# Kernel optimization log

Measured on AMD Instinct MI355X. Metric: run time of the kernel, lower is better.

Reference implementation:

```python
import jax, jax.numpy as jnp
import numpy as np

N, E, IN, HID, HEADS, EDIM, LAT = 10000, 160000, 20, 256, 4, 3, 1024


def gat(x, ei, ea, W, a_src, a_dst, We, a_e, b, H, C):
    # PyG GATConv, eval mode. ei: [2,E], ea: [E,edge_dim]
    n = x.shape[0]
    s, d = ei[0], ei[1]
    # add_self_loops with fill_value='mean': self-loop attr = mean of incoming edge attrs
    cnt = jax.ops.segment_sum(jnp.ones_like(s, jnp.float32), d, num_segments=n)
    loop_ea = jax.ops.segment_sum(ea, d, num_segments=n) / jnp.maximum(cnt, 1.0)[:, None]
    ar = jnp.arange(n, dtype=s.dtype)
    s = jnp.concatenate([s, ar])
    d = jnp.concatenate([d, ar])
    ea = jnp.concatenate([ea, loop_ea], axis=0)
    h = (x @ W).reshape(n, H, C)                       # [n,H,C]
    al_s = jnp.einsum('nhc,hc->nh', h, a_src)
    al_d = jnp.einsum('nhc,hc->nh', h, a_dst)
    e = (ea @ We).reshape(-1, H, C)                    # [E',H,C]
    al_e = jnp.einsum('ehc,hc->eh', e, a_e)
    alpha = jax.nn.leaky_relu(al_s[s] + al_d[d] + al_e, 0.2)  # [E',H]
    m = jax.ops.segment_max(alpha, d, num_segments=n)
    ex = jnp.exp(alpha - m[d])
    ssum = jax.ops.segment_sum(ex, d, num_segments=n)
    alpha = ex / (ssum[d] + 1e-16)
    out = jax.ops.segment_sum(h[s] * alpha[:, :, None], d, num_segments=n)
    return out.reshape(n, H * C) + b


def ln(x, g, b, eps=1e-5):
    m = x.mean(-1, keepdims=True)
    v = ((x - m) ** 2).mean(-1, keepdims=True)
    return g * (x - m) / jnp.sqrt(v + eps) + b


def setup_inputs() -> dict:
    key = jax.random.key(0)
    ks = jax.random.split(key, 16)
    sc = 0.05
    HC = HID * HEADS  # 1024
    return {
        'x': jax.random.normal(ks[0], (N, IN), jnp.float32),
        'edge_attr': jax.random.normal(ks[1], (E, EDIM), jnp.float32),
        'W1': jax.random.normal(ks[2], (IN, HC), jnp.float32) * sc,
        'a_src1': jax.random.normal(ks[3], (HEADS, HID), jnp.float32) * sc,
        'a_dst1': jax.random.normal(ks[4], (HEADS, HID), jnp.float32) * sc,
        'We1': jax.random.normal(ks[5], (EDIM, HC), jnp.float32) * sc,
        'a_e1': jax.random.normal(ks[6], (HEADS, HID), jnp.float32) * sc,
        'b1': jnp.zeros((HC,), jnp.float32),
        'g1': jnp.ones((HC,), jnp.float32),
        'be1': jnp.zeros((HC,), jnp.float32),
        'W2': jax.random.normal(ks[7], (HC, HID), jnp.float32) * sc,
        'a_src2': jax.random.normal(ks[8], (1, HID), jnp.float32) * sc,
        'a_dst2': jax.random.normal(ks[9], (1, HID), jnp.float32) * sc,
        'We2': jax.random.normal(ks[10], (EDIM, HID), jnp.float32) * sc,
        'a_e2': jax.random.normal(ks[11], (1, HID), jnp.float32) * sc,
        'b2': jnp.zeros((HID,), jnp.float32),
        'g2': jnp.ones((HID,), jnp.float32),
        'be2': jnp.zeros((HID,), jnp.float32),
        'Wfc': jax.random.normal(ks[12], (2 * HID, LAT), jnp.float32) * sc,
        'bfc': jnp.zeros((LAT,), jnp.float32),
        'gf': jnp.ones((LAT,), jnp.float32),
        'bf': jnp.zeros((LAT,), jnp.float32),
        'edge_index': jax.random.randint(ks[13], (2, E), 0, N, jnp.int32),
    }


def reference(x, edge_attr, W1, a_src1, a_dst1, We1, a_e1, b1, g1, be1,
              W2, a_src2, a_dst2, We2, a_e2, b2, g2, be2,
              Wfc, bfc, gf, bf, edge_index):
    h = jax.nn.elu(gat(x, edge_index, edge_attr, W1, a_src1, a_dst1, We1, a_e1, b1, HEADS, HID))
    h = ln(h, g1, be1)
    h = jax.nn.elu(gat(h, edge_index, edge_attr, W2, a_src2, a_dst2, We2, a_e2, b2, 1, HID))
    h = ln(h, g2, be2)
    x_mean = h.mean(axis=0)   # global_mean_pool, batch all zeros
    x_max = h.max(axis=0)     # global_max_pool
    g = jnp.concatenate([x_mean, x_max])[None, :]  # [1, 2*HID]
    out = ln(jax.nn.relu(g @ Wfc + bfc), gf, bf)   # [1, LAT]
    return out
```

## Files before the change

kernel.cpp:

```cpp
#include <hip/hip_runtime.h>
#include <hip/hip_bf16.h>

#define NN   10000
#define NE   160000
#define NEP  170000
#define IND  20
#define HIDD 256
#define NH   4
#define HCD  1024
#define LATD 1024
#define MPAD 10112
#define NREP 32

typedef __attribute__((ext_vector_type(8))) short short8v;
typedef __attribute__((ext_vector_type(4))) float f32x4;

__device__ __forceinline__ unsigned pk2(float a, float b) {
    union { __hip_bfloat16 h; unsigned short s; } x, y;
    x.h = __float2bfloat16(a); y.h = __float2bfloat16(b);
    return (unsigned)x.s | ((unsigned)y.s << 16);
}

__device__ __forceinline__ float block_reduce_sum1(float v, float* sm) {
    #pragma unroll
    for (int o = 32; o > 0; o >>= 1) v += __shfl_xor(v, o, 64);
    int wid = threadIdx.x >> 6, lane = threadIdx.x & 63, nw = blockDim.x >> 6;
    if (lane == 0) sm[wid] = v;
    __syncthreads();
    float r = 0.f;
    for (int i = 0; i < nw; i++) r += sm[i];
    __syncthreads();
    return r;
}

__global__ void k_prep(const float* __restrict__ W1, const float* __restrict__ as1,
                       const float* __restrict__ ad1, const float* __restrict__ We1,
                       const float* __restrict__ ae1, const float* __restrict__ We2,
                       const float* __restrict__ ae2, const float* __restrict__ W2,
                       float* __restrict__ prm, __hip_bfloat16* __restrict__ Bt,
                       __hip_bfloat16* __restrict__ w1b) {
    int bid = blockIdx.x, t = threadIdx.x;
    if (bid < 64) {
        __shared__ float sm[64][65];
        int k0 = (bid & 15) * 64, c0 = (bid >> 4) * 64;
        #pragma unroll
        for (int i = 0; i < 16; i++) {
            int idx = i * 256 + t;
            int r = idx >> 6, c = idx & 63;
            sm[r][c] = W2[(size_t)(k0 + r) * 256 + c0 + c];
        }
        __syncthreads();
        int c = t >> 2, kq = t & 3;
        unsigned int out[8];
        #pragma unroll
        for (int j = 0; j < 8; j++)
            out[j] = pk2(sm[kq * 16 + 2*j][c], sm[kq * 16 + 2*j + 1][c]);
        unsigned int* dst = (unsigned int*)(Bt + (size_t)(c0 + c) * 1024 + k0 + kq * 16);
        *(uint4*)dst = make_uint4(out[0], out[1], out[2], out[3]);
        *(uint4*)(dst + 4) = make_uint4(out[4], out[5], out[6], out[7]);
    } else if (bid == 64) {
        if (t < 80) {
            int i = t >> 2, h = t & 3; float s = 0.f;
            for (int c = 0; c < HIDD; c++) s += W1[i*HCD + h*HIDD + c] * as1[h*HIDD + c];
            prm[t] = s;
        } else if (t < 160) {
            int u = t - 80; int i = u >> 2, h = u & 3; float s = 0.f;
            for (int c = 0; c < HIDD; c++) s += W1[i*HCD + h*HIDD + c] * ad1[h*HIDD + c];
            prm[t] = s;
        } else if (t < 172) {
            int u = t - 160; int j = u >> 2, h = u & 3; float s = 0.f;
            for (int c = 0; c < HIDD; c++) s += We1[j*HCD + h*HIDD + c] * ae1[h*HIDD + c];
            prm[t] = s;
        } else if (t < 175) {
            int j = t - 172; float s = 0.f;
            for (int c = 0; c < HIDD; c++) s += We2[j*HIDD + c] * ae2[c];
            prm[t] = s;
        }
    } else {
        int base = (bid - 65) * 2560;
        #pragma unroll
        for (int r = 0; r < 10; r++) {
            int id = base + r * 256 + t;
            w1b[id] = __float2bfloat16(W1[id]);
        }
    }
}

__global__ void k_pre1(const int* __restrict__ ei, const float* __restrict__ ea,
                       const float* __restrict__ x, const float* __restrict__ prm,
                       float* __restrict__ cnt, float* __restrict__ lea3,
                       float* __restrict__ al1) {
    int e = blockIdx.x * 256 + threadIdx.x;
    if (e < NE) {
        int d = ei[NE + e];
        atomicAdd(&cnt[d], 1.0f);
        atomicAdd(&lea3[d*3+0], ea[e*3+0]);
        atomicAdd(&lea3[d*3+1], ea[e*3+1]);
        atomicAdd(&lea3[d*3+2], ea[e*3+2]);
    }
    if (e < NN) {
        int v = e;
        float xr[IND];
        #pragma unroll
        for (int i = 0; i < IND; i++) xr[i] = x[v * IND + i];
        #pragma unroll
        for (int h = 0; h < NH; h++) {
            float s = 0.f, d2 = 0.f;
            #pragma unroll
            for (int i = 0; i < IND; i++) { s += xr[i] * prm[i*4 + h]; d2 += xr[i] * prm[80 + i*4 + h]; }
            al1[v*8 + h] = s;
            al1[v*8 + 4 + h] = d2;
        }
    }
}

__global__ void k_scan(const float* __restrict__ cnt, int* __restrict__ offs) {
    __shared__ int sm[1024];
    int t = threadIdx.x;
    int base = t * 10;
    int loc[10]; int s = 0;
    if (t < 1000) {
        #pragma unroll
        for (int i = 0; i < 10; i++) { loc[i] = s; s += (int)cnt[base + i] + 1; }
    }
    sm[t] = (t < 1000) ? s : 0;
    __syncthreads();
    for (int o = 1; o < 1024; o <<= 1) {
        int x = (t >= o) ? sm[t - o] : 0;
        __syncthreads();
        sm[t] += x;
        __syncthreads();
    }
    int pre = (t > 0) ? sm[t - 1] : 0;
    if (t < 1000) {
        #pragma unroll
        for (int i = 0; i < 10; i++) offs[base + i] = pre + loc[i];
    }
    if (t == 1023) offs[NN] = sm[1023];
}

__global__ void k_edge1(const int* __restrict__ ei, const float* __restrict__ ea,
                        const float* __restrict__ cnt, const float* __restrict__ lea3,
                        const float* __restrict__ al1, const float* __restrict__ prm,
                        const int* __restrict__ offs, int* __restrict__ fill1,
                        int* __restrict__ csrs, float* __restrict__ cex1,
                        float* __restrict__ elog2) {
    int e = blockIdx.x * 256 + threadIdx.x;
    if (e >= NEP) return;
    int s, d; float e0, e1, e2;
    if (e < NE) {
        s = ei[e]; d = ei[NE + e];
        e0 = ea[e*3]; e1 = ea[e*3+1]; e2 = ea[e*3+2];
    } else {
        int v = e - NE; s = v; d = v;
        float ic = 1.f / fmaxf(cnt[v], 1.0f);
        e0 = lea3[v*3] * ic; e1 = lea3[v*3+1] * ic; e2 = lea3[v*3+2] * ic;
    }
    int slot = offs[d] + atomicAdd(&fill1[d], 1);
    csrs[slot] = s;
    elog2[slot] = e0*prm[172] + e1*prm[173] + e2*prm[174];
    float ex[4];
    #pragma unroll
    for (int h = 0; h < NH; h++) {
        float le = e0 * prm[160 + h] + e1 * prm[164 + h] + e2 * prm[168 + h];
        float lg = al1[s*8 + h] + al1[d*8 + 4 + h] + le;
        lg = lg > 0.f ? lg : 0.2f * lg;
        ex[h] = expf(lg);
    }
    *(float4*)(cex1 + (size_t)slot * 4) = make_float4(ex[0], ex[1], ex[2], ex[3]);
}

__global__ void __launch_bounds__(256)
k_agg1x(const int* __restrict__ offs, const int* __restrict__ csrs,
        const float* __restrict__ cex1, const float* __restrict__ x,
        const __hip_bfloat16* __restrict__ w1b, const float* __restrict__ b1,
        const float* __restrict__ g1, const float* __restrict__ be1,
        __hip_bfloat16* __restrict__ h1b) {
    __shared__ float xs[4][4][20];
    int l = threadIdx.x & 63, wid = threadIdx.x >> 6;
    int v = blockIdx.x * 4 + wid;
    int beg = offs[v], end = offs[v + 1];
    int half = l >> 5, lx = l & 31;
    float4 ps = make_float4(0.f, 0.f, 0.f, 0.f);
    float ac0 = 0.f, ac1 = 0.f, ac2 = 0.f, ac3 = 0.f;
    for (int j = beg; j < end; j += 64) {
        int nb = end - j; if (nb > 64) nb = 64;
        int jl = j + l;
        bool valid = jl < end;
        int sidx = csrs[valid ? jl : (end - 1)];
        float4 av = valid ? *(const float4*)(cex1 + (size_t)jl * 4)
                          : make_float4(0.f, 0.f, 0.f, 0.f);
        ps.x += av.x; ps.y += av.y; ps.z += av.z; ps.w += av.w;
        for (int u = 0; u < nb; u += 2) {
            int e = u + half;
            int s  = __shfl(sidx, e, 64);
            float w0 = __shfl(av.x, e, 64);
            float w1v = __shfl(av.y, e, 64);
            float w2 = __shfl(av.z, e, 64);
            float w3 = __shfl(av.w, e, 64);
            float xv = (lx < IND) ? x[(size_t)s * IND + lx] : 0.f;
            ac0 += w0 * xv; ac1 += w1v * xv; ac2 += w2 * xv; ac3 += w3 * xv;
        }
    }
    ac0 += __shfl_xor(ac0, 32, 64);
    ac1 += __shfl_xor(ac1, 32, 64);
    ac2 += __shfl_xor(ac2, 32, 64);
    ac3 += __shfl_xor(ac3, 32, 64);
    #pragma unroll
    for (int o = 1; o <= 32; o <<= 1) {
        ps.x += __shfl_xor(ps.x, o, 64);
        ps.y += __shfl_xor(ps.y, o, 64);
        ps.z += __shfl_xor(ps.z, o, 64);
        ps.w += __shfl_xor(ps.w, o, 64);
    }
    if (l < IND) {
        xs[wid][0][l] = ac0; xs[wid][1][l] = ac1;
        xs[wid][2][l] = ac2; xs[wid][3][l] = ac3;
    }
    __syncthreads();
    int hh = l >> 4;
    float invh = 1.f / ((hh == 0 ? ps.x : hh == 1 ? ps.y : hh == 2 ? ps.z : ps.w) + 1e-16f);
    float xreg[IND];
    #pragma unroll
    for (int i = 0; i < IND; i++) xreg[i] = xs[wid][hh][i];
    float vv[16];
    #pragma unroll
    for (int c = 0; c < 16; c++) vv[c] = 0.f;
    #pragma unroll
    for (int i = 0; i < IND; i++) {
        const uint4* wp = (const uint4*)(w1b + (size_t)i * HCD + 16 * l);
        uint4 wa = wp[0], wb = wp[1];
        float xi = xreg[i];
        unsigned wd[8] = {wa.x, wa.y, wa.z, wa.w, wb.x, wb.y, wb.z, wb.w};
        #pragma unroll
        for (int q = 0; q < 8; q++) {
            vv[2*q]   += xi * __uint_as_float(wd[q] << 16);
            vv[2*q+1] += xi * __uint_as_float(wd[q] & 0xffff0000u);
        }
    }
    const float4* b4 = (const float4*)(b1 + 16 * l);
    float lsum = 0.f;
    #pragma unroll
    for (int q = 0; q < 4; q++) {
        float4 bb = b4[q];
        float xv;
        xv = vv[4*q+0] * invh + bb.x; xv = xv > 0.f ? xv : expm1f(xv); vv[4*q+0] = xv; lsum += xv;
        xv = vv[4*q+1] * invh + bb.y; xv = xv > 0.f ? xv : expm1f(xv); vv[4*q+1] = xv; lsum += xv;
        xv = vv[4*q+2] * invh + bb.z; xv = xv > 0.f ? xv : expm1f(xv); vv[4*q+2] = xv; lsum += xv;
        xv = vv[4*q+3] * invh + bb.w; xv = xv > 0.f ? xv : expm1f(xv); vv[4*q+3] = xv; lsum += xv;
    }
    #pragma unroll
    for (int o = 1; o <= 32; o <<= 1) lsum += __shfl_xor(lsum, o, 64);
    float mu = lsum * (1.f / 1024.f);
    float q2 = 0.f;
    #pragma unroll
    for (int i = 0; i < 16; i++) { float dv = vv[i] - mu; q2 += dv * dv; }
    #pragma unroll
    for (int o = 1; o <= 32; o <<= 1) q2 += __shfl_xor(q2, o, 64);
    float rstd = rsqrtf(q2 * (1.f / 1024.f) + 1e-5f);
    const float4* g4 = (const float4*)(g1 + 16 * l);
    const float4* e4 = (const float4*)(be1 + 16 * l);
    unsigned ou[8];
    #pragma unroll
    for (int q = 0; q < 4; q++) {
        float4 gg = g4[q], ee = e4[q];
        float y0 = gg.x * (vv[4*q+0] - mu) * rstd + ee.x;
        float y1 = gg.y * (vv[4*q+1] - mu) * rstd + ee.y;
        float y2 = gg.z * (vv[4*q+2] - mu) * rstd + ee.z;
        float y3 = gg.w * (vv[4*q+3] - mu) * rstd + ee.w;
        ou[2*q]   = pk2(y0, y1);
        ou[2*q+1] = pk2(y2, y3);
    }
    uint4* dst = (uint4*)(h1b + (size_t)v * HCD + 16 * l);
    dst[0] = make_uint4(ou[0], ou[1], ou[2], ou[3]);
    dst[1] = make_uint4(ou[4], ou[5], ou[6], ou[7]);
}

__global__ void __launch_bounds__(256)
k_gemm2m(const __hip_bfloat16* __restrict__ A, const __hip_bfloat16* __restrict__ Bt,
         __hip_bfloat16* __restrict__ h2b) {
    __shared__ uint4 As4[256];
    char* As = (char*)As4;
    int t = threadIdx.x, l = t & 63, w = t >> 6;
    int m0 = blockIdx.x * 32;
    int srow = t >> 3, skc = t & 7;
    const __hip_bfloat16* gA = A + (size_t)(m0 + srow) * 1024 + skc * 8;
    int wbyte = (srow * 128 + skc * 16) ^ ((srow & 7) << 4);
    int r0 = l & 15, g = l >> 4;
    int ra[2][2];
    #pragma unroll
    for (int m = 0; m < 2; m++)
        #pragma unroll
        for (int kk = 0; kk < 2; kk++) {
            int r = r0 + m * 16;
            ra[m][kk] = (r * 128 + kk * 64 + g * 16) ^ ((r & 7) << 4);
        }
    const __hip_bfloat16* gB = Bt + (size_t)(w * 64 + r0) * 1024 + g * 8;
    f32x4 acc[2][4];
    #pragma unroll
    for (int m = 0; m < 2; m++)
        #pragma unroll
        for (int n = 0; n < 4; n++) acc[m][n] = (f32x4){0.f,0.f,0.f,0.f};
    uint4 sreg = *(const uint4*)gA;
    for (int it = 0; it < 16; ++it) {
        *(uint4*)(As + wbyte) = sreg;
        __syncthreads();
        if (it < 15) sreg = *(const uint4*)(gA + (it + 1) * 64);
        int k0 = it * 64;
        short8v bfr[4][2];
        #pragma unroll
        for (int n = 0; n < 4; n++)
            #pragma unroll
            for (int kk = 0; kk < 2; kk++)
                bfr[n][kk] = *(const short8v*)(gB + (size_t)n * 16 * 1024 + k0 + kk * 32);
        short8v afr[2][2];
        #pragma unroll
        for (int m = 0; m < 2; m++)
            #pragma unroll
            for (int kk = 0; kk < 2; kk++)
                afr[m][kk] = *(const short8v*)(As + ra[m][kk]);
        #pragma unroll
        for (int kk = 0; kk < 2; kk++)
            #pragma unroll
            for (int m = 0; m < 2; m++)
                #pragma unroll
                for (int n = 0; n < 4; n++)
                    acc[m][n] = __builtin_amdgcn_mfma_f32_16x16x32_bf16(afr[m][kk], bfr[n][kk], acc[m][n], 0, 0, 0);
        __syncthreads();
    }
    #pragma unroll
    for (int m = 0; m < 2; m++) {
        #pragma unroll
        for (int r = 0; r < 4; r++) {
            int row = m0 + m * 16 + g * 4 + r;
            if (row < NN) {
                #pragma unroll
                for (int n = 0; n < 4; n++) {
                    int col = w * 64 + n * 16 + r0;
                    h2b[(size_t)row * HIDD + col] = __float2bfloat16(acc[m][n][r]);
                }
            }
        }
    }
}

__global__ void __launch_bounds__(256)
k_al2(const __hip_bfloat16* __restrict__ h2b, const float* __restrict__ as2,
      const float* __restrict__ ad2, float* __restrict__ al2) {
    int l = threadIdx.x & 63;
    int v = blockIdx.x * 4 + (threadIdx.x >> 6);
    uint2 p = ((const uint2*)h2b)[(size_t)v * 64 + l];
    float f0 = __uint_as_float(p.x << 16), f1 = __uint_as_float(p.x & 0xffff0000u);
    float f2 = __uint_as_float(p.y << 16), f3 = __uint_as_float(p.y & 0xffff0000u);
    float4 sa = ((const float4*)as2)[l];
    float4 da = ((const float4*)ad2)[l];
    float s = f0*sa.x + f1*sa.y + f2*sa.z + f3*sa.w;
    float d = f0*da.x + f1*da.y + f2*da.z + f3*da.w;
    #pragma unroll
    for (int o = 1; o <= 32; o <<= 1) { s += __shfl_xor(s, o, 64); d += __shfl_xor(d, o, 64); }
    if (l == 0) { al2[v*2] = s; al2[v*2+1] = d; }
}

__global__ void __launch_bounds__(256)
k_agg2(const int* __restrict__ offs, const int* __restrict__ csrs,
       const float* __restrict__ elog2, const float* __restrict__ al2,
       const __hip_bfloat16* __restrict__ h2b, const float* __restrict__ b2,
       const float* __restrict__ g2, const float* __restrict__ be2,
       float* __restrict__ gsum, unsigned* __restrict__ gmaxU) {
    __shared__ float smS[4][256];
    int l = threadIdx.x & 63, w = threadIdx.x >> 6;
    int v = blockIdx.x * 4 + w;
    int beg = offs[v], end = offs[v + 1];
    float ald = al2[2*v + 1];
    float a0 = 0.f, a1 = 0.f, a2 = 0.f, a3 = 0.f, ps = 0.f;
    const uint2* hU = (const uint2*)h2b;
    for (int j = beg; j < end; j += 64) {
        int nb = end - j; if (nb > 64) nb = 64;
        int jl = j + l;
        bool valid = jl < end;
        int sidx = csrs[valid ? jl : (end - 1)];
        float wv = 0.f;
        if (valid) {
            float lg = al2[2*sidx] + ald + elog2[jl];
            lg = lg > 0.f ? lg : 0.2f * lg;
            wv = expf(lg);
        }
        ps += wv;
        for (int u = 0; u < nb; u += 2) {
            int s0 = __shfl(sidx, u, 64);
            int s1 = __shfl(sidx, u + 1, 64);
            float w0 = __shfl(wv, u, 64);
            float w1 = __shfl(wv, u + 1, 64);
            uint2 p = hU[(size_t)s0 * 64 + l];
            uint2 q = hU[(size_t)s1 * 64 + l];
            a0 += w0 * __uint_as_float(p.x << 16);
            a1 += w0 * __uint_as_float(p.x & 0xffff0000u);
            a2 += w0 * __uint_as_float(p.y << 16);
            a3 += w0 * __uint_as_float(p.y & 0xffff0000u);
            a0 += w1 * __uint_as_float(q.x << 16);
            a1 += w1 * __uint_as_float(q.x & 0xffff0000u);
            a2 += w1 * __uint_as_float(q.y << 16);
            a3 += w1 * __uint_as_float(q.y & 0xffff0000u);
        }
    }
    #pragma unroll
    for (int o = 1; o <= 32; o <<= 1) ps += __shfl_xor(ps, o, 64);
    float inv = 1.f / (ps + 1e-16f);
    float4 bb = ((const float4*)b2)[l];
    float v0 = a0 * inv + bb.x, v1 = a1 * inv + bb.y, v2 = a2 * inv + bb.z, v3 = a3 * inv + bb.w;
    v0 = v0 > 0.f ? v0 : expm1f(v0);
    v1 = v1 > 0.f ? v1 : expm1f(v1);
    v2 = v2 > 0.f ? v2 : expm1f(v2);
    v3 = v3 > 0.f ? v3 : expm1f(v3);
    float lsum = v0 + v1 + v2 + v3;
    #pragma unroll
    for (int o = 1; o <= 32; o <<= 1) lsum += __shfl_xor(lsum, o, 64);
    float mu = lsum * (1.f / 256.f);
    float q2 = (v0-mu)*(v0-mu) + (v1-mu)*(v1-mu) + (v2-mu)*(v2-mu) + (v3-mu)*(v3-mu);
    #pragma unroll
    for (int o = 1; o <= 32; o <<= 1) q2 += __shfl_xor(q2, o, 64);
    float rstd = rsqrtf(q2 * (1.f / 256.f) + 1e-5f);
    float4 gg = ((const float4*)g2)[l];
    float4 ee = ((const float4*)be2)[l];
    float4 outv;
    outv.x = gg.x * (v0 - mu) * rstd + ee.x;
    outv.y = gg.y * (v1 - mu) * rstd + ee.y;
    outv.z = gg.z * (v2 - mu) * rstd + ee.z;
    outv.w = gg.w * (v3 - mu) * rstd + ee.w;
    *((float4*)&smS[w][4 * l]) = outv;
    __syncthreads();
    int t = threadIdx.x;
    int rep = blockIdx.x & (NREP - 1);
    float s = smS[0][t] + smS[1][t] + smS[2][t] + smS[3][t];
    float m = fmaxf(fmaxf(smS[0][t], smS[1][t]), fmaxf(smS[2][t], smS[3][t]));
    atomicAdd(&gsum[rep * 256 + t], s);
    unsigned b = __float_as_uint(m);
    unsigned k = (b & 0x80000000u) ? ~b : (b | 0x80000000u);
    atomicMax(&gmaxU[rep * 256 + t], k);
}

__global__ void k_gvec(const float* __restrict__ gsum, const unsigned* __restrict__ gmaxU,
                       float* __restrict__ gvec) {
    int t = threadIdx.x;
    float s = 0.f; unsigned km = 0u;
    #pragma unroll
    for (int r = 0; r < NREP; r++) {
        s += gsum[r * 256 + t];
        unsigned k = gmaxU[r * 256 + t];
        km = k > km ? k : km;
    }
    gvec[t] = s * (1.f / (float)NN);
    unsigned b = (km & 0x80000000u) ? (km & 0x7fffffffu) : ~km;
    gvec[256 + t] = __uint_as_float(b);
}

__global__ void k_fc(const float* __restrict__ gvec, const float* __restrict__ Wfc,
                     const float* __restrict__ bfc, float* __restrict__ fcp) {
    int c = blockIdx.x * 128 + threadIdx.x;
    float acc = bfc[c];
    for (int i = 0; i < 512; i++) acc += gvec[i] * Wfc[i * LATD + c];
    fcp[c] = fmaxf(acc, 0.f);
}

__global__ void k_out(const float* __restrict__ fcp, const float* __restrict__ gf,
                      const float* __restrict__ bf, float* __restrict__ outp) {
    __shared__ float sm[16];
    int t = threadIdx.x;
    float v = fcp[t];
    float mu = block_reduce_sum1(v, sm) * (1.f / 1024.f);
    float dv = v - mu;
    float var = block_reduce_sum1(dv * dv, sm) * (1.f / 1024.f);
    float rstd = rsqrtf(var + 1e-5f);
    outp[t] = gf[t] * dv * rstd + bf[t];
}

extern "C" void kernel_launch(void* const* d_in, const int* in_sizes, int n_in,
                              void* d_out, int out_size, void* d_ws, size_t ws_size,
                              hipStream_t stream) {
    const float* x      = (const float*)d_in[0];
    const float* ea     = (const float*)d_in[1];
    const float* W1     = (const float*)d_in[2];
    const float* a_src1 = (const float*)d_in[3];
    const float* a_dst1 = (const float*)d_in[4];
    const float* We1    = (const float*)d_in[5];
    const float* a_e1   = (const float*)d_in[6];
    const float* b1     = (const float*)d_in[7];
    const float* g1     = (const float*)d_in[8];
    const float* be1    = (const float*)d_in[9];
    const float* W2     = (const float*)d_in[10];
    const float* a_src2 = (const float*)d_in[11];
    const float* a_dst2 = (const float*)d_in[12];
    const float* We2    = (const float*)d_in[13];
    const float* a_e2   = (const float*)d_in[14];
    const float* b2     = (const float*)d_in[15];
    const float* g2     = (const float*)d_in[16];
    const float* be2    = (const float*)d_in[17];
    const float* Wfc    = (const float*)d_in[18];
    const float* bfc    = (const float*)d_in[19];
    const float* gf     = (const float*)d_in[20];
    const float* bf     = (const float*)d_in[21];
    const int*   ei     = (const int*)d_in[22];
    float* outp = (float*)d_out;

    char* p = (char*)d_ws;
    auto alloc = [&](size_t bytes) -> char* {
        char* r = p;
        p += (bytes + 255) & ~(size_t)255;
        return r;
    };
    float* cnt     = (float*)alloc((size_t)NN * 4);
    float* lea3    = (float*)alloc((size_t)NN * 3 * 4);
    int*   fill1   = (int*)  alloc((size_t)NN * 4);
    float* gsum    = (float*)alloc((size_t)NREP * 256 * 4);
    unsigned* gmaxU= (unsigned*)alloc((size_t)NREP * 256 * 4);
    size_t zbytes  = (size_t)((char*)gmaxU + (size_t)NREP*256*4 - (char*)cnt);
    float* prm     = (float*)alloc(256 * 4);
    float* al1     = (float*)alloc((size_t)NN * 8 * 4);
    float* al2     = (float*)alloc((size_t)NN * 2 * 4);
    int*   offs    = (int*)  alloc((size_t)(NN + 1) * 4);
    int*   csrs    = (int*)  alloc((size_t)NEP * 4);
    float* cex1    = (float*)alloc((size_t)NEP * 4 * 4);
    float* elog2   = (float*)alloc((size_t)NEP * 4);
    __hip_bfloat16* w1b = (__hip_bfloat16*)alloc((size_t)IND * HCD * 2);
    __hip_bfloat16* h1b = (__hip_bfloat16*)alloc((size_t)MPAD * HCD * 2);
    __hip_bfloat16* w2t = (__hip_bfloat16*)alloc((size_t)HIDD * HCD * 2);
    __hip_bfloat16* h2b = (__hip_bfloat16*)alloc((size_t)NN * HIDD * 2);
    float* gvec    = (float*)alloc(512 * 4);
    float* fcp     = (float*)alloc(1024 * 4);

    hipMemsetAsync(cnt, 0, zbytes, stream);

    k_prep<<<73, 256, 0, stream>>>(W1, a_src1, a_dst1, We1, a_e1, We2, a_e2, W2,
                                   prm, w2t, w1b);
    k_pre1<<<(NE + 255) / 256, 256, 0, stream>>>(ei, ea, x, prm, cnt, lea3, al1);
    k_scan<<<1, 1024, 0, stream>>>(cnt, offs);
    k_edge1<<<(NEP + 255) / 256, 256, 0, stream>>>(ei, ea, cnt, lea3, al1, prm, offs,
                                                   fill1, csrs, cex1, elog2);
    k_agg1x<<<NN / 4, 256, 0, stream>>>(offs, csrs, cex1, x, w1b, b1, g1, be1, h1b);
    k_gemm2m<<<313, 256, 0, stream>>>(h1b, w2t, h2b);
    k_al2<<<NN / 4, 256, 0, stream>>>(h2b, a_src2, a_dst2, al2);
    k_agg2<<<NN / 4, 256, 0, stream>>>(offs, csrs, elog2, al2, h2b, b2, g2, be2,
                                       gsum, gmaxU);
    k_gvec<<<1, 256, 0, stream>>>(gsum, gmaxU, gvec);
    k_fc<<<8, 128, 0, stream>>>(gvec, Wfc, bfc, fcp);
    k_out<<<1, 1024, 0, stream>>>(fcp, gf, bf, outp);
}
```

Baseline: 318.2 us.

## Restructure layer aggregations and split final FC across blocks

Layer-1 aggregation now gathers neighbor features with 8 edges per wave in parallel and has each block compute the 20x1024 projection for 4 nodes sharing the same weight loads. Layer-2 aggregation uses one 256-thread block per node, staging edge weights and indices in shared memory. Global pooling atomics are spread over more replicas to cut contention. The final FC is split along K across 32 blocks with atomic accumulation, moving bias and ReLU into the output kernel. This trades more blocks and more block-level syncs for better parallelism and reuse.

```diff
diff --git a/kernel.cpp b/kernel.cpp
--- a/kernel.cpp
+++ b/kernel.cpp
@@ -10,7 +10,7 @@
 #define HCD  1024
 #define LATD 1024
 #define MPAD 10112
-#define NREP 32
+#define NREP 128
 
 typedef __attribute__((ext_vector_type(8))) short short8v;
 typedef __attribute__((ext_vector_type(4))) float f32x4;
@@ -31,6 +31,25 @@
     for (int i = 0; i < nw; i++) r += sm[i];
     __syncthreads();
     return r;
+}
+
+__device__ __forceinline__ void block_reduce_sum4(float* v, float* sm) {
+    #pragma unroll
+    for (int h = 0; h < 4; h++) {
+        #pragma unroll
+        for (int o = 32; o > 0; o >>= 1) v[h] += __shfl_xor(v[h], o, 64);
+    }
+    int wid = threadIdx.x >> 6, lane = threadIdx.x & 63, nw = blockDim.x >> 6;
+    if (lane == 0) {
+        sm[wid*4+0] = v[0]; sm[wid*4+1] = v[1]; sm[wid*4+2] = v[2]; sm[wid*4+3] = v[3];
+    }
+    __syncthreads();
+    float r[4] = {0.f, 0.f, 0.f, 0.f};
+    for (int i = 0; i < nw; i++) {
+        r[0] += sm[i*4+0]; r[1] += sm[i*4+1]; r[2] += sm[i*4+2]; r[3] += sm[i*4+3];
+    }
+    __syncthreads();
+    v[0] = r[0]; v[1] = r[1]; v[2] = r[2]; v[3] = r[3];
 }
 
 __global__ void k_prep(const float* __restrict__ W1, const float* __restrict__ as1,
@@ -171,109 +190,106 @@
 }
 
 __global__ void __launch_bounds__(256)
-k_agg1x(const int* __restrict__ offs, const int* __restrict__ csrs,
+k_agg1y(const int* __restrict__ offs, const int* __restrict__ csrs,
         const float* __restrict__ cex1, const float* __restrict__ x,
         const __hip_bfloat16* __restrict__ w1b, const float* __restrict__ b1,
         const float* __restrict__ g1, const float* __restrict__ be1,
         __hip_bfloat16* __restrict__ h1b) {
-    __shared__ float xs[4][4][20];
-    int l = threadIdx.x & 63, wid = threadIdx.x >> 6;
-    int v = blockIdx.x * 4 + wid;
-    int beg = offs[v], end = offs[v + 1];
-    int half = l >> 5, lx = l & 31;
-    float4 ps = make_float4(0.f, 0.f, 0.f, 0.f);
-    float ac0 = 0.f, ac1 = 0.f, ac2 = 0.f, ac3 = 0.f;
-    for (int j = beg; j < end; j += 64) {
-        int nb = end - j; if (nb > 64) nb = 64;
-        int jl = j + l;
-        bool valid = jl < end;
-        int sidx = csrs[valid ? jl : (end - 1)];
-        float4 av = valid ? *(const float4*)(cex1 + (size_t)jl * 4)
-                          : make_float4(0.f, 0.f, 0.f, 0.f);
-        ps.x += av.x; ps.y += av.y; ps.z += av.z; ps.w += av.w;
-        for (int u = 0; u < nb; u += 2) {
-            int e = u + half;
-            int s  = __shfl(sidx, e, 64);
-            float w0 = __shfl(av.x, e, 64);
-            float w1v = __shfl(av.y, e, 64);
-            float w2 = __shfl(av.z, e, 64);
-            float w3 = __shfl(av.w, e, 64);
-            float xv = (lx < IND) ? x[(size_t)s * IND + lx] : 0.f;
-            ac0 += w0 * xv; ac1 += w1v * xv; ac2 += w2 * xv; ac3 += w3 * xv;
-        }
-    }
-    ac0 += __shfl_xor(ac0, 32, 64);
-    ac1 += __shfl_xor(ac1, 32, 64);
-    ac2 += __shfl_xor(ac2, 32, 64);
-    ac3 += __shfl_xor(ac3, 32, 64);
-    #pragma unroll
-    for (int o = 1; o <= 32; o <<= 1) {
-        ps.x += __shfl_xor(ps.x, o, 64);
-        ps.y += __shfl_xor(ps.y, o, 64);
-        ps.z += __shfl_xor(ps.z, o, 64);
-        ps.w += __shfl_xor(ps.w, o, 64);
-    }
-    if (l < IND) {
-        xs[wid][0][l] = ac0; xs[wid][1][l] = ac1;
-        xs[wid][2][l] = ac2; xs[wid][3][l] = ac3;
+    __shared__ float xsn[4][NH][20];
+    __shared__ float smr[16];
+    int t = threadIdx.x, l = t & 63, n0 = t >> 6;
+    int v4 = blockIdx.x * 4;
+    {
+        int v = v4 + n0;
+        int beg = offs[v], end = offs[v + 1];
+        int e = l >> 3, fs = l & 7;
+        float acc[4][3] = {{0.f,0.f,0.f},{0.f,0.f,0.f},{0.f,0.f,0.f},{0.f,0.f,0.f}};
+        float psa[4] = {0.f, 0.f, 0.f, 0.f};
+        for (int j0 = beg; j0 < end; j0 += 8) {
+            int jl = j0 + e;
+            bool valid = jl < end;
+            int s = csrs[valid ? jl : beg];
+            float4 a4 = valid ? *(const float4*)(cex1 + (size_t)jl * 4)
+                              : make_float4(0.f, 0.f, 0.f, 0.f);
+            psa[0] += a4.x; psa[1] += a4.y; psa[2] += a4.z; psa[3] += a4.w;
+            #pragma unroll
+            for (int k = 0; k < 3; k++) {
+                int fi = fs * 3 + k;
+                float xv = (fi < IND) ? x[(size_t)s * IND + fi] : 0.f;
+                acc[0][k] += a4.x * xv; acc[1][k] += a4.y * xv;
+                acc[2][k] += a4.z * xv; acc[3][k] += a4.w * xv;
+            }
+        }
+        #pragma unroll
+        for (int o = 8; o <= 32; o <<= 1) {
+            #pragma unroll
+            for (int h = 0; h < 4; h++) {
+                psa[h] += __shfl_xor(psa[h], o, 64);
+                #pragma unroll
+                for (int k = 0; k < 3; k++) acc[h][k] += __shfl_xor(acc[h][k], o, 64);
+            }
+        }
+        if (e == 0) {
+            #pragma unroll
+            for (int h = 0; h < 4; h++) {
+                float inv = 1.f / (psa[h] + 1e-16f);
+                #pragma unroll
+                for (int k = 0; k < 3; k++) {
+                    int fi = fs * 3 + k;
+                    if (fi < IND) xsn[n0][h][fi] = acc[h][k] * inv;
+                }
+            }
+        }
     }
     __syncthreads();
-    int hh = l >> 4;
-    float invh = 1.f / ((hh == 0 ? ps.x : hh == 1 ? ps.y : hh == 2 ? ps.z : ps.w) + 1e-16f);
-    float xreg[IND];
-    #pragma unroll
-    for (int i = 0; i < IND; i++) xreg[i] = xs[wid][hh][i];
-    float vv[16];
-    #pragma unroll
-    for (int c = 0; c < 16; c++) vv[c] = 0.f;
+    int hh = t >> 6;
+    float vv[4][4] = {{0.f,0.f,0.f,0.f},{0.f,0.f,0.f,0.f},{0.f,0.f,0.f,0.f},{0.f,0.f,0.f,0.f}};
     #pragma unroll
     for (int i = 0; i < IND; i++) {
-        const uint4* wp = (const uint4*)(w1b + (size_t)i * HCD + 16 * l);
-        uint4 wa = wp[0], wb = wp[1];
-        float xi = xreg[i];
-        unsigned wd[8] = {wa.x, wa.y, wa.z, wa.w, wb.x, wb.y, wb.z, wb.w};
-        #pragma unroll
-        for (int q = 0; q < 8; q++) {
-            vv[2*q]   += xi * __uint_as_float(wd[q] << 16);
-            vv[2*q+1] += xi * __uint_as_float(wd[q] & 0xffff0000u);
-        }
-    }
-    const float4* b4 = (const float4*)(b1 + 16 * l);
-    float lsum = 0.f;
-    #pragma unroll
-    for (int q = 0; q < 4; q++) {
-        float4 bb = b4[q];
-        float xv;
-        xv = vv[4*q+0] * invh + bb.x; xv = xv > 0.f ? xv : expm1f(xv); vv[4*q+0] = xv; lsum += xv;
-        xv = vv[4*q+1] * invh + bb.y; xv = xv > 0.f ? xv : expm1f(xv); vv[4*q+1] = xv; lsum += xv;
-        xv = vv[4*q+2] * invh + bb.z; xv = xv > 0.f ? xv : expm1f(xv); vv[4*q+2] = xv; lsum += xv;
-        xv = vv[4*q+3] * invh + bb.w; xv = xv > 0.f ? xv : expm1f(xv); vv[4*q+3] = xv; lsum += xv;
-    }
-    #pragma unroll
-    for (int o = 1; o <= 32; o <<= 1) lsum += __shfl_xor(lsum, o, 64);
-    float mu = lsum * (1.f / 1024.f);
-    float q2 = 0.f;
-    #pragma unroll
-    for (int i = 0; i < 16; i++) { float dv = vv[i] - mu; q2 += dv * dv; }
-    #pragma unroll
-    for (int o = 1; o <= 32; o <<= 1) q2 += __shfl_xor(q2, o, 64);
-    float rstd = rsqrtf(q2 * (1.f / 1024.f) + 1e-5f);
-    const float4* g4 = (const float4*)(g1 + 16 * l);
-    const float4* e4 = (const float4*)(be1 + 16 * l);
-    unsigned ou[8];
-    #pragma unroll
-    for (int q = 0; q < 4; q++) {
-        float4 gg = g4[q], ee = e4[q];
-        float y0 = gg.x * (vv[4*q+0] - mu) * rstd + ee.x;
-        float y1 = gg.y * (vv[4*q+1] - mu) * rstd + ee.y;
-        float y2 = gg.z * (vv[4*q+2] - mu) * rstd + ee.z;
-        float y3 = gg.w * (vv[4*q+3] - mu) * rstd + ee.w;
-        ou[2*q]   = pk2(y0, y1);
-        ou[2*q+1] = pk2(y2, y3);
-    }
-    uint4* dst = (uint4*)(h1b + (size_t)v * HCD + 16 * l);
-    dst[0] = make_uint4(ou[0], ou[1], ou[2], ou[3]);
-    dst[1] = make_uint4(ou[4], ou[5], ou[6], ou[7]);
+        uint2 wd = *(const uint2*)(w1b + (size_t)i * HCD + 4 * t);
+        float w0 = __uint_as_float(wd.x << 16);
+        float w1 = __uint_as_float(wd.x & 0xffff0000u);
+        float w2 = __uint_as_float(wd.y << 16);
+        float w3 = __uint_as_float(wd.y & 0xffff0000u);
+        #pragma unroll
+        for (int n = 0; n < 4; n++) {
+            float xi = xsn[n][hh][i];
+            vv[n][0] += xi * w0; vv[n][1] += xi * w1;
+            vv[n][2] += xi * w2; vv[n][3] += xi * w3;
+        }
+    }
+    float4 bb = ((const float4*)b1)[t];
+    float ls[4];
+    #pragma unroll
+    for (int n = 0; n < 4; n++) {
+        float s0, s1, s2, s3;
+        s0 = vv[n][0] + bb.x; s0 = s0 > 0.f ? s0 : expm1f(s0);
+        s1 = vv[n][1] + bb.y; s1 = s1 > 0.f ? s1 : expm1f(s1);
+        s2 = vv[n][2] + bb.z; s2 = s2 > 0.f ? s2 : expm1f(s2);
+        s3 = vv[n][3] + bb.w; s3 = s3 > 0.f ? s3 : expm1f(s3);
+        vv[n][0] = s0; vv[n][1] = s1; vv[n][2] = s2; vv[n][3] = s3;
+        ls[n] = s0 + s1 + s2 + s3;
+    }
+    block_reduce_sum4(ls, smr);
+    float mu[4], q2[4];
+    #pragma unroll
+    for (int n = 0; n < 4; n++) {
+        mu[n] = ls[n] * (1.f / 1024.f);
+        float d0 = vv[n][0]-mu[n], d1 = vv[n][1]-mu[n], d2 = vv[n][2]-mu[n], d3 = vv[n][3]-mu[n];
+        q2[n] = d0*d0 + d1*d1 + d2*d2 + d3*d3;
+    }
+    block_reduce_sum4(q2, smr);
+    float4 gg = ((const float4*)g1)[t];
+    float4 ee = ((const float4*)be1)[t];
+    #pragma unroll
+    for (int n = 0; n < 4; n++) {
+        float rstd = rsqrtf(q2[n] * (1.f / 1024.f) + 1e-5f);
+        float y0 = gg.x * (vv[n][0] - mu[n]) * rstd + ee.x;
+        float y1 = gg.y * (vv[n][1] - mu[n]) * rstd + ee.y;
+        float y2 = gg.z * (vv[n][2] - mu[n]) * rstd + ee.z;
+        float y3 = gg.w * (vv[n][3] - mu[n]) * rstd + ee.w;
+        *(uint2*)(h1b + (size_t)(v4 + n) * HCD + 4 * t) = make_uint2(pk2(y0, y1), pk2(y2, y3));
+    }
 }
 
 __global__ void __launch_bounds__(256)
@@ -362,79 +378,58 @@
 }
 
 __global__ void __launch_bounds__(256)
-k_agg2(const int* __restrict__ offs, const int* __restrict__ csrs,
-       const float* __restrict__ elog2, const float* __restrict__ al2,
-       const __hip_bfloat16* __restrict__ h2b, const float* __restrict__ b2,
-       const float* __restrict__ g2, const float* __restrict__ be2,
-       float* __restrict__ gsum, unsigned* __restrict__ gmaxU) {
-    __shared__ float smS[4][256];
-    int l = threadIdx.x & 63, w = threadIdx.x >> 6;
-    int v = blockIdx.x * 4 + w;
+k_agg2y(const int* __restrict__ offs, const int* __restrict__ csrs,
+        const float* __restrict__ elog2, const float* __restrict__ al2,
+        const __hip_bfloat16* __restrict__ h2b, const float* __restrict__ b2,
+        const float* __restrict__ g2, const float* __restrict__ be2,
+        float* __restrict__ gsum, unsigned* __restrict__ gmaxU) {
+    __shared__ float sal[128];
+    __shared__ int   ssr[128];
+    __shared__ float sred[16];
+    int t = threadIdx.x;
+    int v = blockIdx.x;
     int beg = offs[v], end = offs[v + 1];
-    float ald = al2[2*v + 1];
-    float a0 = 0.f, a1 = 0.f, a2 = 0.f, a3 = 0.f, ps = 0.f;
-    const uint2* hU = (const uint2*)h2b;
-    for (int j = beg; j < end; j += 64) {
-        int nb = end - j; if (nb > 64) nb = 64;
-        int jl = j + l;
-        bool valid = jl < end;
-        int sidx = csrs[valid ? jl : (end - 1)];
-        float wv = 0.f;
-        if (valid) {
-            float lg = al2[2*sidx] + ald + elog2[jl];
-            lg = lg > 0.f ? lg : 0.2f * lg;
-            wv = expf(lg);
-        }
-        ps += wv;
-        for (int u = 0; u < nb; u += 2) {
-            int s0 = __shfl(sidx, u, 64);
-            int s1 = __shfl(sidx, u + 1, 64);
-            float w0 = __shfl(wv, u, 64);
-            float w1 = __shfl(wv, u + 1, 64);
-            uint2 p = hU[(size_t)s0 * 64 + l];
-            uint2 q = hU[(size_t)s1 * 64 + l];
-            a0 += w0 * __uint_as_float(p.x << 16);
-            a1 += w0 * __uint_as_float(p.x & 0xffff0000u);
-            a2 += w0 * __uint_as_float(p.y << 16);
-            a3 += w0 * __uint_as_float(p.y & 0xffff0000u);
-            a0 += w1 * __uint_as_float(q.x << 16);
-            a1 += w1 * __uint_as_float(q.x & 0xffff0000u);
-            a2 += w1 * __uint_as_float(q.y << 16);
-            a3 += w1 * __uint_as_float(q.y & 0xffff0000u);
-        }
-    }
-    #pragma unroll
-    for (int o = 1; o <= 32; o <<= 1) ps += __shfl_xor(ps, o, 64);
-    float inv = 1.f / (ps + 1e-16f);
-    float4 bb = ((const float4*)b2)[l];
-    float v0 = a0 * inv + bb.x, v1 = a1 * inv + bb.y, v2 = a2 * inv + bb.z, v3 = a3 * inv + bb.w;
-    v0 = v0 > 0.f ? v0 : expm1f(v0);
-    v1 = v1 > 0.f ? v1 : expm1f(v1);
-    v2 = v2 > 0.f ? v2 : expm1f(v2);
-    v3 = v3 > 0.f ? v3 : expm1f(v3);
-    float lsum = v0 + v1 + v2 + v3;
-    #pragma unroll
-    for (int o = 1; o <= 32; o <<= 1) lsum += __shfl_xor(lsum, o, 64);
-    float mu = lsum * (1.f / 256.f);
-    float q2 = (v0-mu)*(v0-mu) + (v1-mu)*(v1-mu) + (v2-mu)*(v2-mu) + (v3-mu)*(v3-mu);
-    #pragma unroll
-    for (int o = 1; o <= 32; o <<= 1) q2 += __shfl_xor(q2, o, 64);
-    float rstd = rsqrtf(q2 * (1.f / 256.f) + 1e-5f);
-    float4 gg = ((const float4*)g2)[l];
-    float4 ee = ((const float4*)be2)[l];
-    float4 outv;
-    outv.x = gg.x * (v0 - mu) * rstd + ee.x;
-    outv.y = gg.y * (v1 - mu) * rstd + ee.y;
-    outv.z = gg.z * (v2 - mu) * rstd + ee.z;
-    outv.w = gg.w * (v3 - mu) * rstd + ee.w;
-    *((float4*)&smS[w][4 * l]) = outv;
-    __syncthreads();
-    int t = threadIdx.x;
+    float ald = al2[2 * v + 1];
+    float acc = 0.f, ps = 0.f;
+    for (int j0 = beg; j0 < end; j0 += 128) {
+        int nb = end - j0; if (nb > 128) nb = 128;
+        __syncthreads();
+        if (t < 128) {
+            int jl = j0 + t;
+            float wv = 0.f; int s = 0;
+            if (jl < end) {
+                s = csrs[jl];
+                float lg = al2[2 * s] + ald + elog2[jl];
+                lg = lg > 0.f ? lg : 0.2f * lg;
+                wv = expf(lg);
+            }
+            sal[t] = wv; ssr[t] = s;
+            ps += wv;
+        }
+        __syncthreads();
+        int nbr = (nb + 3) & ~3;
+        for (int u = 0; u < nbr; u += 4) {
+            float a0 = sal[u], a1 = sal[u+1], a2 = sal[u+2], a3 = sal[u+3];
+            int s0 = ssr[u], s1 = ssr[u+1], s2 = ssr[u+2], s3 = ssr[u+3];
+            float h0 = __bfloat162float(h2b[(size_t)s0 * HIDD + t]);
+            float h1 = __bfloat162float(h2b[(size_t)s1 * HIDD + t]);
+            float h2 = __bfloat162float(h2b[(size_t)s2 * HIDD + t]);
+            float h3 = __bfloat162float(h2b[(size_t)s3 * HIDD + t]);
+            acc += a0*h0 + a1*h1 + a2*h2 + a3*h3;
+        }
+    }
+    float pst = block_reduce_sum1(ps, sred);
+    float inv = 1.f / (pst + 1e-16f);
+    float vf = acc * inv + b2[t];
+    vf = vf > 0.f ? vf : expm1f(vf);
+    float mu = block_reduce_sum1(vf, sred) * (1.f / 256.f);
+    float dv = vf - mu;
+    float var = block_reduce_sum1(dv * dv, sred) * (1.f / 256.f);
+    float rstd = rsqrtf(var + 1e-5f);
+    float outv = g2[t] * dv * rstd + be2[t];
     int rep = blockIdx.x & (NREP - 1);
-    float s = smS[0][t] + smS[1][t] + smS[2][t] + smS[3][t];
-    float m = fmaxf(fmaxf(smS[0][t], smS[1][t]), fmaxf(smS[2][t], smS[3][t]));
-    atomicAdd(&gsum[rep * 256 + t], s);
-    unsigned b = __float_as_uint(m);
+    atomicAdd(&gsum[rep * 256 + t], outv);
+    unsigned b = __float_as_uint(outv);
     unsigned k = (b & 0x80000000u) ? ~b : (b | 0x80000000u);
     atomicMax(&gmaxU[rep * 256 + t], k);
 }
@@ -443,7 +438,6 @@
                        float* __restrict__ gvec) {
     int t = threadIdx.x;
     float s = 0.f; unsigned km = 0u;
-    #pragma unroll
     for (int r = 0; r < NREP; r++) {
         s += gsum[r * 256 + t];
         unsigned k = gmaxU[r * 256 + t];
@@ -455,18 +449,23 @@
 }
 
 __global__ void k_fc(const float* __restrict__ gvec, const float* __restrict__ Wfc,
-                     const float* __restrict__ bfc, float* __restrict__ fcp) {
-    int c = blockIdx.x * 128 + threadIdx.x;
-    float acc = bfc[c];
-    for (int i = 0; i < 512; i++) acc += gvec[i] * Wfc[i * LATD + c];
-    fcp[c] = fmaxf(acc, 0.f);
-}
-
-__global__ void k_out(const float* __restrict__ fcp, const float* __restrict__ gf,
-                      const float* __restrict__ bf, float* __restrict__ outp) {
+                     float* __restrict__ fcacc) {
+    int t = threadIdx.x;
+    int kc = blockIdx.x >> 2;
+    int c = (blockIdx.x & 3) * 256 + t;
+    int r0 = kc * 64;
+    float acc = 0.f;
+    #pragma unroll 8
+    for (int i = 0; i < 64; i++) acc += gvec[r0 + i] * Wfc[(size_t)(r0 + i) * LATD + c];
+    atomicAdd(&fcacc[c], acc);
+}
+
+__global__ void k_out(const float* __restrict__ fcacc, const float* __restrict__ bfc,
+                      const float* __restrict__ gf, const float* __restrict__ bf,
+                      float* __restrict__ outp) {
     __shared__ float sm[16];
     int t = threadIdx.x;
-    float v = fcp[t];
+    float v = fmaxf(fcacc[t] + bfc[t], 0.f);
     float mu = block_reduce_sum1(v, sm) * (1.f / 1024.f);
     float dv = v - mu;
     float var = block_reduce_sum1(dv * dv, sm) * (1.f / 1024.f);
@@ -513,7 +512,8 @@
     int*   fill1   = (int*)  alloc((size_t)NN * 4);
     float* gsum    = (float*)alloc((size_t)NREP * 256 * 4);
     unsigned* gmaxU= (unsigned*)alloc((size_t)NREP * 256 * 4);
-    size_t zbytes  = (size_t)((char*)gmaxU + (size_t)NREP*256*4 - (char*)cnt);
+    float* fcacc   = (float*)alloc(1024 * 4);
+    size_t zbytes  = (size_t)((char*)fcacc + 1024*4 - (char*)cnt);
     float* prm     = (float*)alloc(256 * 4);
     float* al1     = (float*)alloc((size_t)NN * 8 * 4);
     float* al2     = (float*)alloc((size_t)NN * 2 * 4);
@@ -526,7 +526,6 @@
     __hip_bfloat16* w2t = (__hip_bfloat16*)alloc((size_t)HIDD * HCD * 2);
     __hip_bfloat16* h2b = (__hip_bfloat16*)alloc((size_t)NN * HIDD * 2);
     float* gvec    = (float*)alloc(512 * 4);
-    float* fcp     = (float*)alloc(1024 * 4);
 
     hipMemsetAsync(cnt, 0, zbytes, stream);
 
@@ -536,12 +535,12 @@
     k_scan<<<1, 1024, 0, stream>>>(cnt, offs);
     k_edge1<<<(NEP + 255) / 256, 256, 0, stream>>>(ei, ea, cnt, lea3, al1, prm, offs,
                                                    fill1, csrs, cex1, elog2);
-    k_agg1x<<<NN / 4, 256, 0, stream>>>(offs, csrs, cex1, x, w1b, b1, g1, be1, h1b);
+    k_agg1y<<<NN / 4, 256, 0, stream>>>(offs, csrs, cex1, x, w1b, b1, g1, be1, h1b);
     k_gemm2m<<<313, 256, 0, stream>>>(h1b, w2t, h2b);
     k_al2<<<NN / 4, 256, 0, stream>>>(h2b, a_src2, a_dst2, al2);
-    k_agg2<<<NN / 4, 256, 0, stream>>>(offs, csrs, elog2, al2, h2b, b2, g2, be2,
-                                       gsum, gmaxU);
+    k_agg2y<<<NN, 256, 0, stream>>>(offs, csrs, elog2, al2, h2b, b2, g2, be2,
+                                    gsum, gmaxU);
     k_gvec<<<1, 256, 0, stream>>>(gsum, gmaxU, gvec);
-    k_fc<<<8, 128, 0, stream>>>(gvec, Wfc, bfc, fcp);
-    k_out<<<1, 1024, 0, stream>>>(fcp, gf, bf, outp);
-}
+    k_fc<<<32, 256, 0, stream>>>(gvec, Wfc, fcacc);
+    k_out<<<1, 1024, 0, stream>>>(fcacc, bfc, gf, bf, outp);
+}
```

New measurement: 305.5 us. 1.04x faster.
